# Performance work log

Hardware: AMD Instinct MI355X
Metric: run time of the kernel (lower is better)

## Reference

```python
import jax, jax.numpy as jnp
import numpy as np

N, E, D, L = 100000, 400000, 300, 5
BN_EPS = 1e-5


def setup_inputs() -> dict:
    key = jax.random.key(0)
    ks = jax.random.split(key, 8)
    x = jax.random.randint(ks[0], (N, 7), 0, 5)
    edge_index = jax.random.randint(ks[1], (2, E), 0, N)
    edge_attr = jax.random.randint(ks[2], (E, 4), 0, 2)
    s = 0.1
    atom_tables = jax.random.normal(ks[3], (7, 119, D), jnp.float32) * s
    bond_tables = jax.random.normal(ks[4], (L, 4, 6, D), jnp.float32) * s
    mlp_w1 = jax.random.normal(ks[5], (L, D, 2 * D), jnp.float32) * (1.0 / np.sqrt(D))
    mlp_b1 = jnp.zeros((L, 2 * D), jnp.float32)
    mlp_w2 = jax.random.normal(ks[6], (L, 2 * D, D), jnp.float32) * (1.0 / np.sqrt(2 * D))
    mlp_b2 = jnp.zeros((L, D), jnp.float32)
    bn_gamma = jnp.ones((L, D), jnp.float32)
    bn_beta = jnp.zeros((L, D), jnp.float32)
    return dict(x=x, edge_index=edge_index, edge_attr=edge_attr,
                atom_tables=atom_tables, bond_tables=bond_tables,
                mlp_w1=mlp_w1, mlp_b1=mlp_b1, mlp_w2=mlp_w2, mlp_b2=mlp_b2,
                bn_gamma=bn_gamma, bn_beta=bn_beta)


def reference(x, edge_index, edge_attr, atom_tables, bond_tables,
              mlp_w1, mlp_b1, mlp_w2, mlp_b2, bn_gamma, bn_beta):
    n = x.shape[0]
    # add self loops (PyG add_self_loops appends them)
    loop = jnp.arange(n)
    src = jnp.concatenate([edge_index[0], loop])  # message source j
    dst = jnp.concatenate([edge_index[1], loop])  # aggregation target i
    self_loop_attr = jnp.zeros((n, 4), edge_attr.dtype).at[:, 0].set(4)
    ea = jnp.concatenate([edge_attr, self_loop_attr], axis=0)  # [E+N, 4]

    # AtomEncoder: sum of 7 per-feature embeddings -> [N, D]
    h = atom_tables[jnp.arange(7), x].sum(axis=1)

    for l in range(L):
        # BondEncoder: sum of 4 per-feature embeddings -> [E+N, D]
        e_emb = bond_tables[l][jnp.arange(4), ea].sum(axis=1)
        # GIN message = x_j + edge_emb, aggr='add' by target node
        msg = h[src] + e_emb
        agg = jax.ops.segment_sum(msg, dst, num_segments=n)
        # GIN update MLP: Linear -> ReLU -> Linear
        hid = jax.nn.relu(agg @ mlp_w1[l] + mlp_b1[l])
        out = hid @ mlp_w2[l] + mlp_b2[l]
        # BatchNorm1d (training mode: batch stats, biased var)
        mu = out.mean(axis=0)
        var = out.var(axis=0)
        out = (out - mu) / jnp.sqrt(var + BN_EPS) * bn_gamma[l] + bn_beta[l]
        # drop_ratio = 0.0 -> dropout is identity; ReLU except last layer
        if l < L - 1:
            out = jax.nn.relu(out)
        h = out
    return h  # JK='last'
```

## Files before the change

### kernel.cpp

```cpp
#include <hip/hip_runtime.h>

typedef unsigned short u16;
typedef unsigned int   u32;
typedef __bf16 bf16x8 __attribute__((ext_vector_type(8)));
typedef float  f32x4  __attribute__((ext_vector_type(4)));

__device__ __forceinline__ u16 f2bf(float f) {
    u32 u = __builtin_bit_cast(u32, f);
    u = u + 0x7fffu + ((u >> 16) & 1u);
    return (u16)(u >> 16);
}
__device__ __forceinline__ float bflo(u32 u) { return __builtin_bit_cast(float, u << 16); }
__device__ __forceinline__ float bfhi(u32 u) { return __builtin_bit_cast(float, u & 0xffff0000u); }
__device__ __forceinline__ u32 pack2(float x, float y) { return (u32)f2bf(x) | ((u32)f2bf(y) << 16); }

__device__ __forceinline__ void gll16(const u16* g, u16* l) {
    __builtin_amdgcn_global_load_lds(
        (const __attribute__((address_space(1))) void*)g,
        (__attribute__((address_space(3))) void*)l, 16, 0, 0);
}

#define NN 100000
#define EE 400000
#define DP 320
#define HP 640

__global__ void count_deg(const int* __restrict__ ei, int* __restrict__ deg, int E) {
    int e = blockIdx.x * 256 + threadIdx.x;
    if (e < E) atomicAdd(&deg[ei[E + e]], 1);
}

__global__ void scan1(const int* __restrict__ deg, int* __restrict__ out, int* __restrict__ bsums, int n) {
    __shared__ int lds[1024];
    int t = threadIdx.x;
    int i = blockIdx.x * 1024 + t;
    int v = (i < n) ? deg[i] : 0;
    lds[t] = v;
    __syncthreads();
    for (int d = 1; d < 1024; d <<= 1) {
        int add = (t >= d) ? lds[t - d] : 0;
        __syncthreads();
        lds[t] += add;
        __syncthreads();
    }
    if (i < n) out[i] = lds[t] - v;
    if (t == 1023) bsums[blockIdx.x] = lds[t];
}

__global__ void scan2(int* __restrict__ bsums, int nb) {
    __shared__ int lds[128];
    int t = threadIdx.x;
    int v = (t < nb) ? bsums[t] : 0;
    lds[t] = v;
    __syncthreads();
    for (int d = 1; d < 128; d <<= 1) {
        int add = (t >= d) ? lds[t - d] : 0;
        __syncthreads();
        lds[t] += add;
        __syncthreads();
    }
    if (t < nb) bsums[t] = lds[t] - v;
}

__global__ void scan3(int* __restrict__ out, const int* __restrict__ bsums, int n, int etot) {
    int i = blockIdx.x * 1024 + threadIdx.x;
    if (i < n) out[i] += bsums[blockIdx.x];
    else if (i == n) out[i] = etot;
}

__global__ void fill_csr(const int* __restrict__ ei, const int* __restrict__ ea,
                         int* __restrict__ cursors, u32* __restrict__ vals, int E) {
    int e = blockIdx.x * 256 + threadIdx.x;
    if (e >= E) return;
    int dst = ei[E + e];
    int src = ei[e];
    u32 code = (u32)((ea[e*4] & 1) | ((ea[e*4+1] & 1) << 1) | ((ea[e*4+2] & 1) << 2) | ((ea[e*4+3] & 1) << 3));
    int pos = atomicAdd(&cursors[dst], 1);
    vals[pos] = ((u32)src << 4) | code;
}

__global__ void conv_w1(const float* __restrict__ w, u16* __restrict__ wt) {
    int id = blockIdx.x * 256 + threadIdx.x;
    if (id >= 5 * HP * DP) return;
    int l = id / (HP * DP);
    int rem = id - l * (HP * DP);
    int n = rem / DP;
    int kidx = rem - n * DP;
    int u = kidx >> 3, e = kidx & 7;
    int kk = ((u ^ (n & 7)) << 3) | e;
    u16 v = 0;
    if (n < 600 && kk < 300) v = f2bf(w[((size_t)l * 300 + kk) * 600 + n]);
    wt[id] = v;
}
__global__ void conv_w2(const float* __restrict__ w, u16* __restrict__ wt) {
    int id = blockIdx.x * 256 + threadIdx.x;
    if (id >= 5 * DP * HP) return;
    int l = id / (DP * HP);
    int rem = id - l * (DP * HP);
    int n = rem / HP;
    int kp = rem - n * HP;
    int up = kp >> 3, e = kp & 7;
    int ul = (up & ~3) | ((up & 3) ^ ((n >> 1) & 3));
    int kk = (ul << 3) | e;
    u16 v = 0;
    if (n < 300 && kk < 600) v = f2bf(w[((size_t)l * 600 + kk) * 300 + n]);
    wt[id] = v;
}

__global__ void atom_enc(const int* __restrict__ x, const float* __restrict__ at, u16* __restrict__ y) {
    const int i = blockIdx.x;
    const int d = threadIdx.x;
    __shared__ int xi[7];
    if (d < 7) xi[d] = x[i * 7 + d];
    __syncthreads();
    u16 v = 0;
    if (d < 300) {
        float s = 0.f;
        #pragma unroll
        for (int f = 0; f < 7; ++f) s += at[(f * 119 + xi[f]) * 300 + d];
        v = f2bf(s);
    }
    y[(size_t)i * DP + d] = v;
}

__global__ void bond_enc(const float* __restrict__ bt, float* __restrict__ emb) {
    const int c = blockIdx.x;
    const int d = threadIdx.x;
    float s = 0.f;
    if (d < 300) {
        if (c < 16) {
            #pragma unroll
            for (int f = 0; f < 4; ++f) s += bt[(f * 6 + ((c >> f) & 1)) * 300 + d];
        } else {
            s = bt[4 * 300 + d];
            #pragma unroll
            for (int f = 1; f < 4; ++f) s += bt[f * 6 * 300 + d];
        }
    }
    emb[c * DP + d] = s;
}

__global__ void bn_ss(const float* __restrict__ stats, const float* __restrict__ gamma,
                      const float* __restrict__ beta, float* __restrict__ scale,
                      float* __restrict__ shift, int n) {
    int d = threadIdx.x;
    float sc = 0.f, sh = 0.f;
    if (d < 300) {
        float inv_n = 1.0f / (float)n;
        float mu = stats[d] * inv_n;
        float var = stats[DP + d] * inv_n - mu * mu;
        float inv = 1.0f / sqrtf(var + 1e-5f);
        sc = gamma[d] * inv;
        sh = beta[d] - mu * sc;
    }
    scale[d] = sc; shift[d] = sh;
}

__global__ void bn_apply(const float* __restrict__ hraw, const float* __restrict__ scale,
                         const float* __restrict__ shift, u16* __restrict__ y) {
    const int i = blockIdx.x;
    const int d = threadIdx.x;
    float v = fmaf(scale[d], hraw[(size_t)i * DP + d], shift[d]);
    y[(size_t)i * DP + d] = f2bf(fmaxf(v, 0.f));
}

__global__ void aggregate(const u16* __restrict__ y,
                          const float* __restrict__ emb,
                          const int* __restrict__ offs, const u32* __restrict__ vals,
                          u16* __restrict__ agg, const int n) {
    const int wid = (int)((blockIdx.x * (size_t)blockDim.x + threadIdx.x) >> 6);
    const int lane = threadIdx.x & 63;
    if (wid >= n) return;
    const bool act = (lane < 40);

    float acc[8];
    #pragma unroll
    for (int i = 0; i < 8; ++i) acc[i] = 0.f;

    auto accum = [&](int srcrow, const float* erow) {
        if (act) {
            uint4 v = *(const uint4*)(y + (size_t)srcrow * DP + lane * 8);
            float4 e0 = *(const float4*)(erow + lane * 8);
            float4 e1 = *(const float4*)(erow + lane * 8 + 4);
            acc[0] += bflo(v.x) + e0.x;  acc[1] += bfhi(v.x) + e0.y;
            acc[2] += bflo(v.y) + e0.z;  acc[3] += bfhi(v.y) + e0.w;
            acc[4] += bflo(v.z) + e1.x;  acc[5] += bfhi(v.z) + e1.y;
            acc[6] += bflo(v.w) + e1.z;  acc[7] += bfhi(v.w) + e1.w;
        }
    };

    accum(wid, emb + 16 * DP);
    const int s = offs[wid], t = offs[wid + 1];
    for (int e = s; e < t; ++e) {
        u32 v = vals[e];
        accum((int)(v >> 4), emb + (v & 15u) * DP);
    }

    if (act) {
        uint4 o;
        o.x = pack2(acc[0], acc[1]);
        o.y = pack2(acc[2], acc[3]);
        o.z = pack2(acc[4], acc[5]);
        o.w = pack2(acc[6], acc[7]);
        *(uint4*)(agg + (size_t)wid * DP + lane * 8) = o;
    }
}

__global__ __launch_bounds__(512, 2) void fused_mlp(
    const u16* __restrict__ A,
    const u16* __restrict__ W1t,
    const u16* __restrict__ W2t,
    const float* __restrict__ b1g,
    const float* __restrict__ b2g,
    float* __restrict__ H,
    float* __restrict__ st1, float* __restrict__ st2,
    const int M) {

    __shared__ __align__(16) u16 W1s[2][32 * 320];
    __shared__ __align__(16) u16 W2s[2][320 * 32];
    __shared__ __align__(16) float hidF[2][128 * 36];

    const int tid  = threadIdx.x;
    const int bm   = blockIdx.x * 128;
    const int wave = tid >> 6;
    const int lane = tid & 63;
    const int mg   = wave >> 1;
    const int ng   = wave & 1;
    const int l15  = lane & 15;
    const int q    = lane >> 4;
    const int r7   = l15 & 7;
    const int s2   = (l15 >> 1) & 3;

    for (int i = wave; i < 20; i += 8)
        gll16(W1t + (size_t)(i * 64 + lane) * 8, &W1s[0][i * 512]);

    bf16x8 afr[2][10];
    #pragma unroll
    for (int mf = 0; mf < 2; ++mf) {
        int arow = bm + mg * 32 + mf * 16 + l15;
        if (arow > M - 1) arow = M - 1;
        const u16* ap = A + (size_t)arow * DP + q * 8;
        #pragma unroll
        for (int kt = 0; kt < 10; ++kt)
            afr[mf][kt] = __builtin_bit_cast(bf16x8, *(const uint4*)(ap + kt * 32));
    }

    f32x4 acc2[2][10];
    const f32x4 zero4 = {0.f, 0.f, 0.f, 0.f};
    #pragma unroll
    for (int mf = 0; mf < 2; ++mf)
        #pragma unroll
        for (int nf = 0; nf < 10; ++nf) acc2[mf][nf] = zero4;

    __syncthreads();

    const int rb = (ng * 16 + l15) * 320;

    for (int c = 0; c < 20; ++c) {
        const int pc = c & 1;

        if (c < 19) {
            const u16* g1 = W1t + (size_t)(c + 1) * 10240;
            for (int i = wave; i < 20; i += 8)
                gll16(g1 + (size_t)(i * 64 + lane) * 8, &W1s[pc ^ 1][i * 512]);
        }
        {
            const u16* g2 = W2t + (size_t)c * 32;
            for (int i = wave; i < 20; i += 8) {
                int u = i * 64 + lane;
                gll16(g2 + (size_t)(u >> 2) * HP + (u & 3) * 8, &W2s[pc][i * 512]);
            }
        }

        __builtin_amdgcn_s_setprio(1);
        if (c > 0) {
            bf16x8 a2[2];
            #pragma unroll
            for (int mf = 0; mf < 2; ++mf) {
                const float* hp = &hidF[pc ^ 1][(mg * 32 + mf * 16 + l15) * 36 + q * 8];
                f32x4 lo = *(const f32x4*)hp;
                f32x4 hi = *(const f32x4*)(hp + 4);
                uint4 w;
                w.x = pack2(lo[0], lo[1]);
                w.y = pack2(lo[2], lo[3]);
                w.z = pack2(hi[0], hi[1]);
                w.w = pack2(hi[2], hi[3]);
                a2[mf] = __builtin_bit_cast(bf16x8, w);
            }
            #pragma unroll
            for (int nf = 0; nf < 10; ++nf) {
                int row = ng * 160 + nf * 16 + l15;
                uint4 t = *(const uint4*)&W2s[pc ^ 1][row * 32 + ((q ^ s2) << 3)];
                bf16x8 b = __builtin_bit_cast(bf16x8, t);
                acc2[0][nf] = __builtin_amdgcn_mfma_f32_16x16x32_bf16(a2[0], b, acc2[0][nf], 0, 0, 0);
                acc2[1][nf] = __builtin_amdgcn_mfma_f32_16x16x32_bf16(a2[1], b, acc2[1][nf], 0, 0, 0);
            }
        }

        f32x4 acc1[2] = {zero4, zero4};
        #pragma unroll
        for (int kt = 0; kt < 10; ++kt) {
            uint4 t = *(const uint4*)&W1s[pc][rb + (((kt * 4 + q) ^ r7) << 3)];
            bf16x8 b = __builtin_bit_cast(bf16x8, t);
            acc1[0] = __builtin_amdgcn_mfma_f32_16x16x32_bf16(afr[0][kt], b, acc1[0], 0, 0, 0);
            acc1[1] = __builtin_amdgcn_mfma_f32_16x16x32_bf16(afr[1][kt], b, acc1[1], 0, 0, 0);
        }
        __builtin_amdgcn_s_setprio(0);
        {
            int gcol = c * 32 + ng * 16 + l15;
            float bb = (gcol < 600) ? b1g[gcol] : 0.f;
            #pragma unroll
            for (int mf = 0; mf < 2; ++mf)
                #pragma unroll
                for (int r = 0; r < 4; ++r)
                    hidF[pc][(mg * 32 + mf * 16 + q * 4 + r) * 36 + ng * 16 + l15] =
                        fmaxf(acc1[mf][r] + bb, 0.f);
        }
        __syncthreads();
    }

    {
        bf16x8 a2[2];
        #pragma unroll
        for (int mf = 0; mf < 2; ++mf) {
            const float* hp = &hidF[1][(mg * 32 + mf * 16 + l15) * 36 + q * 8];
            f32x4 lo = *(const f32x4*)hp;
            f32x4 hi = *(const f32x4*)(hp + 4);
            uint4 w;
            w.x = pack2(lo[0], lo[1]);
            w.y = pack2(lo[2], lo[3]);
            w.z = pack2(hi[0], hi[1]);
            w.w = pack2(hi[2], hi[3]);
            a2[mf] = __builtin_bit_cast(bf16x8, w);
        }
        #pragma unroll
        for (int nf = 0; nf < 10; ++nf) {
            int row = ng * 160 + nf * 16 + l15;
            uint4 t = *(const uint4*)&W2s[1][row * 32 + ((q ^ s2) << 3)];
            bf16x8 b = __builtin_bit_cast(bf16x8, t);
            acc2[0][nf] = __builtin_amdgcn_mfma_f32_16x16x32_bf16(a2[0], b, acc2[0][nf], 0, 0, 0);
            acc2[1][nf] = __builtin_amdgcn_mfma_f32_16x16x32_bf16(a2[1], b, acc2[1][nf], 0, 0, 0);
        }
    }

    #pragma unroll
    for (int nf = 0; nf < 10; ++nf) {
        const int col = ng * 160 + nf * 16 + l15;
        const float bb = (col < 300) ? b2g[col] : 0.f;
        float s1 = 0.f, s2v = 0.f;
        #pragma unroll
        for (int mf = 0; mf < 2; ++mf)
            #pragma unroll
            for (int r = 0; r < 4; ++r) {
                const int row = bm + mg * 32 + mf * 16 + q * 4 + r;
                if (row < M) {
                    float v = acc2[mf][nf][r] + bb;
                    H[(size_t)row * DP + col] = v;
                    s1 += v; s2v += v * v;
                }
            }
        s1 += __shfl_xor(s1, 16); s1 += __shfl_xor(s1, 32);
        s2v += __shfl_xor(s2v, 16); s2v += __shfl_xor(s2v, 32);
        if (q == 0) { atomicAdd(&st1[col], s1); atomicAdd(&st2[col], s2v); }
    }
}

__global__ void finalize(const float* __restrict__ hraw, const float* __restrict__ scale,
                         const float* __restrict__ shift, float* __restrict__ out) {
    const int i = blockIdx.x;
    const int d = threadIdx.x;
    if (d < 300) {
        float x = hraw[(size_t)i * DP + d];
        out[(size_t)i * 300 + d] = fmaf(scale[d], x, shift[d]);
    }
}

extern "C" void kernel_launch(void* const* d_in, const int* in_sizes, int n_in,
                              void* d_out, int out_size, void* d_ws, size_t ws_size,
                              hipStream_t stream) {
    const int N = NN, E = EE, L = 5;
    const int*   x     = (const int*)d_in[0];
    const int*   ei    = (const int*)d_in[1];
    const int*   ea    = (const int*)d_in[2];
    const float* at    = (const float*)d_in[3];
    const float* bt    = (const float*)d_in[4];
    const float* w1    = (const float*)d_in[5];
    const float* b1    = (const float*)d_in[6];
    const float* w2    = (const float*)d_in[7];
    const float* b2    = (const float*)d_in[8];
    const float* gamma = (const float*)d_in[9];
    const float* beta  = (const float*)d_in[10];
    float* out = (float*)d_out;

    char* ws = (char*)d_ws;
    size_t off = 0;
    auto alloc = [&](size_t bytes) { char* p = ws + off; off = (off + bytes + 255) & ~(size_t)255; return p; };
    u16* buf_y    = (u16*)alloc((size_t)N * DP * 2);
    u16* buf_agg  = (u16*)alloc((size_t)N * DP * 2);
    float* buf_h  = (float*)alloc((size_t)N * DP * 4);
    u16* w1t      = (u16*)alloc((size_t)5 * HP * DP * 2);
    u16* w2t      = (u16*)alloc((size_t)5 * DP * HP * 2);
    int* deg      = (int*)alloc((size_t)N * 4);
    int* offs     = (int*)alloc((size_t)(N + 1) * 4);
    int* cursors  = (int*)alloc((size_t)N * 4);
    u32* vals     = (u32*)alloc((size_t)E * 4);
    int* bsums    = (int*)alloc(128 * 4);
    float* emb    = (float*)alloc(17 * DP * 4);
    float* stats  = (float*)alloc(2 * DP * 4);
    float* scale  = (float*)alloc(DP * 4);
    float* shift  = (float*)alloc(DP * 4);

    (void)hipMemsetAsync(deg, 0, (size_t)N * 4, stream);
    count_deg<<<(E + 255) / 256, 256, 0, stream>>>(ei, deg, E);
    const int nb = (N + 1023) / 1024;
    scan1<<<nb, 1024, 0, stream>>>(deg, offs, bsums, N);
    scan2<<<1, 128, 0, stream>>>(bsums, nb);
    scan3<<<(N + 1 + 1023) / 1024, 1024, 0, stream>>>(offs, bsums, N, E);
    (void)hipMemcpyAsync(cursors, offs, (size_t)N * 4, hipMemcpyDeviceToDevice, stream);
    fill_csr<<<(E + 255) / 256, 256, 0, stream>>>(ei, ea, cursors, vals, E);

    conv_w1<<<(5 * HP * DP + 255) / 256, 256, 0, stream>>>(w1, w1t);
    conv_w2<<<(5 * DP * HP + 255) / 256, 256, 0, stream>>>(w2, w2t);

    atom_enc<<<N, DP, 0, stream>>>(x, at, buf_y);

    const int MB = (N + 127) / 128;
    for (int l = 0; l < L; ++l) {
        bond_enc<<<17, DP, 0, stream>>>(bt + (size_t)l * 4 * 6 * 300, emb);
        aggregate<<<(N * 64 + 255) / 256, 256, 0, stream>>>(
            buf_y, emb, offs, vals, buf_agg, N);
        (void)hipMemsetAsync(stats, 0, 2 * DP * 4, stream);
        fused_mlp<<<MB, 512, 0, stream>>>(
            buf_agg,
            w1t + (size_t)l * HP * DP, w2t + (size_t)l * DP * HP,
            b1 + (size_t)l * 600, b2 + (size_t)l * 300,
            buf_h, stats, stats + DP, N);
        bn_ss<<<1, DP, 0, stream>>>(stats, gamma + (size_t)l * 300, beta + (size_t)l * 300, scale, shift, N);
        if (l < L - 1)
            bn_apply<<<N, DP, 0, stream>>>(buf_h, scale, shift, buf_y);
    }
    finalize<<<N, DP, 0, stream>>>(buf_h, scale, shift, out);
}
```

Baseline: 2.153 ms.

## Restructure fused MLP weight prefetch with split-wave loads and manual waitcnt barriers

Splits the weight-staging work so waves 0-3 prefetch the next W1 chunk while waves 4-7 prefetch the W2 chunk for the next iteration, and shifts W2 double-buffering one stage ahead. The end-of-loop __syncthreads is replaced by an explicit s_waitcnt vmcnt(5)/lgkmcnt(0) plus s_barrier at the loop top, so outstanding global-to-LDS loads can stay in flight across the barrier. The first-layer bias is staged once in LDS instead of being read from global memory every chunk. This relies on hand-counted vmcnt values, which are fragile if the compiler issues other vector-memory ops or reorders loads, and W2 for chunk 0 appears to arrive only after one iteration of latency.

```diff
diff --git a/kernel.cpp b/kernel.cpp
--- a/kernel.cpp
+++ b/kernel.cpp
@@ -219,6 +219,7 @@
     __shared__ __align__(16) u16 W1s[2][32 * 320];
     __shared__ __align__(16) u16 W2s[2][320 * 32];
     __shared__ __align__(16) float hidF[2][128 * 36];
+    __shared__ __align__(16) float biasL[640];
 
     const int tid  = threadIdx.x;
     const int bm   = blockIdx.x * 128;
@@ -230,9 +231,21 @@
     const int q    = lane >> 4;
     const int r7   = l15 & 7;
     const int s2   = (l15 >> 1) & 3;
-
-    for (int i = wave; i < 20; i += 8)
-        gll16(W1t + (size_t)(i * 64 + lane) * 8, &W1s[0][i * 512]);
+    const int sb   = wave * 5;
+
+    {
+        biasL[tid] = (tid < 600) ? b1g[tid] : 0.f;
+        int i1 = tid + 512;
+        if (i1 < 640) biasL[i1] = (i1 < 600) ? b1g[i1] : 0.f;
+    }
+
+    if (sb < 20) {
+        #pragma unroll
+        for (int k = 0; k < 5; ++k) {
+            int i = sb + k;
+            gll16(W1t + (size_t)(i * 64 + lane) * 8, &W1s[0][i * 512]);
+        }
+    }
 
     bf16x8 afr[2][10];
     #pragma unroll
@@ -252,6 +265,7 @@
         #pragma unroll
         for (int nf = 0; nf < 10; ++nf) acc2[mf][nf] = zero4;
 
+    asm volatile("s_waitcnt vmcnt(0)" ::: "memory");
     __syncthreads();
 
     const int rb = (ng * 16 + l15) * 320;
@@ -259,16 +273,32 @@
     for (int c = 0; c < 20; ++c) {
         const int pc = c & 1;
 
-        if (c < 19) {
+        if (c) {
+            asm volatile("s_waitcnt vmcnt(5) lgkmcnt(0)" ::: "memory");
+        } else {
+            asm volatile("s_waitcnt lgkmcnt(0)" ::: "memory");
+        }
+        __builtin_amdgcn_s_barrier();
+        __builtin_amdgcn_sched_barrier(0);
+
+        {
             const u16* g1 = W1t + (size_t)(c + 1) * 10240;
-            for (int i = wave; i < 20; i += 8)
-                gll16(g1 + (size_t)(i * 64 + lane) * 8, &W1s[pc ^ 1][i * 512]);
-        }
-        {
             const u16* g2 = W2t + (size_t)c * 32;
-            for (int i = wave; i < 20; i += 8) {
-                int u = i * 64 + lane;
-                gll16(g2 + (size_t)(u >> 2) * HP + (u & 3) * 8, &W2s[pc][i * 512]);
+            if (sb < 20) {
+                if (c < 19) {
+                    #pragma unroll
+                    for (int k = 0; k < 5; ++k) {
+                        int i = sb + k;
+                        gll16(g1 + (size_t)(i * 64 + lane) * 8, &W1s[pc ^ 1][i * 512]);
+                    }
+                }
+            } else {
+                #pragma unroll
+                for (int k = 0; k < 5; ++k) {
+                    int j = sb - 20 + k;
+                    int u = j * 64 + lane;
+                    gll16(g2 + (size_t)(u >> 2) * HP + (u & 3) * 8, &W2s[pc ^ 1][j * 512]);
+                }
             }
         }
 
@@ -290,7 +320,7 @@
             #pragma unroll
             for (int nf = 0; nf < 10; ++nf) {
                 int row = ng * 160 + nf * 16 + l15;
-                uint4 t = *(const uint4*)&W2s[pc ^ 1][row * 32 + ((q ^ s2) << 3)];
+                uint4 t = *(const uint4*)&W2s[pc][row * 32 + ((q ^ s2) << 3)];
                 bf16x8 b = __builtin_bit_cast(bf16x8, t);
                 acc2[0][nf] = __builtin_amdgcn_mfma_f32_16x16x32_bf16(a2[0], b, acc2[0][nf], 0, 0, 0);
                 acc2[1][nf] = __builtin_amdgcn_mfma_f32_16x16x32_bf16(a2[1], b, acc2[1][nf], 0, 0, 0);
@@ -308,7 +338,7 @@
         __builtin_amdgcn_s_setprio(0);
         {
             int gcol = c * 32 + ng * 16 + l15;
-            float bb = (gcol < 600) ? b1g[gcol] : 0.f;
+            float bb = biasL[gcol];
             #pragma unroll
             for (int mf = 0; mf < 2; ++mf)
                 #pragma unroll
@@ -316,9 +346,11 @@
                     hidF[pc][(mg * 32 + mf * 16 + q * 4 + r) * 36 + ng * 16 + l15] =
                         fmaxf(acc1[mf][r] + bb, 0.f);
         }
-        __syncthreads();
-    }
-
+    }
+
+    asm volatile("s_waitcnt vmcnt(0) lgkmcnt(0)" ::: "memory");
+    __builtin_amdgcn_s_barrier();
+    __builtin_amdgcn_sched_barrier(0);
     {
         bf16x8 a2[2];
         #pragma unroll
@@ -336,7 +368,7 @@
         #pragma unroll
         for (int nf = 0; nf < 10; ++nf) {
             int row = ng * 160 + nf * 16 + l15;
-            uint4 t = *(const uint4*)&W2s[1][row * 32 + ((q ^ s2) << 3)];
+            uint4 t = *(const uint4*)&W2s[0][row * 32 + ((q ^ s2) << 3)];
             bf16x8 b = __builtin_bit_cast(bf16x8, t);
             acc2[0][nf] = __builtin_amdgcn_mfma_f32_16x16x32_bf16(a2[0], b, acc2[0][nf], 0, 0, 0);
             acc2[1][nf] = __builtin_amdgcn_mfma_f32_16x16x32_bf16(a2[1], b, acc2[1][nf], 0, 0, 0);
```

Measured after the change: 2.203 ms. 2.3% more time.
